# Performance work log

Hardware: AMD Instinct MI355X
Metric: run time of the kernel (lower is better)

Reference implementation:

```python
import jax, jax.numpy as jnp
import numpy as np

# Module hyperparameters (from init_kwargs)
M = 2049          # NpointsMesh (odd)
TAU = 3e-6        # Gaussian spreading width
XLIMS = (0.0, 1.0)
MU0 = 1.0
L = abs(XLIMS[1] - XLIMS[0])
TWO_PI = 2.0 * np.pi
B, N = 16, 512


def _grids():
    kGrid = jnp.asarray(np.linspace(-(M // 2), M // 2, M), jnp.float32)
    xGrid = jnp.asarray(TWO_PI * np.linspace(XLIMS[0], XLIMS[1], M + 1)[:-1] / L, jnp.float32)
    return kGrid, xGrid


def setup_inputs() -> dict:
    key = jax.random.key(0)
    kx, = jax.random.split(key, 1)
    x = jax.random.uniform(kx, (B, N), dtype=jnp.float32)  # points inside xLims
    kGrid, _ = _grids()
    multRe0 = (4.0 * np.pi / (kGrid ** 2 + MU0 ** 2))[None, :].astype(jnp.float32)
    multRe1 = (4.0 * np.pi / (kGrid ** 2 + 1.0))[None, :].astype(jnp.float32)
    zeros = jnp.zeros((1, M), jnp.float32)
    return {"x": x, "multRe0": multRe0, "multIm0": zeros,
            "multRe1": multRe1, "multIm1": zeros}


def reference(x, multRe0, multIm0, multRe1, multIm1):
    kGrid, xGrid = _grids()
    # Gaussian spreading: (B, N, M)
    diff = x[..., None] * (TWO_PI / L) - xGrid
    g = jnp.exp(-(diff * diff) / (4.0 * TAU))
    red = jnp.sum(g, axis=1)  # (B, M)
    # NOTE: tf.signal.fftshift/ifftshift default to ALL axes; jnp matches that default.
    fftG = jnp.fft.fftshift(jnp.fft.fft(jax.lax.complex(red, jnp.zeros_like(red)))) * (L / TWO_PI)
    deconv = jnp.sqrt(np.pi / TAU) * jnp.exp((kGrid ** 2) * TAU)  # (M,) real
    rfft = fftG * deconv
    Re, Im = jnp.real(rfft), jnp.imag(rfft)

    def mix(mRe, mIm):
        # Faithful to source (incl. its naming quirk): real = mRe*Re - mRe*Im,
        # imag = mIm*Re + mIm*Im
        return jax.lax.complex(mRe * Re - mRe * Im, mIm * Re + mIm * Im)

    multFFT = jnp.stack([mix(multRe0, multIm0), mix(multRe1, multIm1)], axis=1)  # (B, 2, M)
    multDeconv = multFFT * deconv  # broadcast over (B, 2, M)
    irfft = jnp.real(jnp.fft.ifft(jnp.fft.ifftshift(multDeconv)))  # (B, 2, M)
    # local = irfft[:,None,:,:] * g[:,:,None,:]; fmm = sum over mesh / M  -> einsum
    fmm = jnp.einsum('bnm,bcm->bnc', g, irfft) / M  # (B, N, 2)
    return fmm
```

## Files before the change

kernel.cpp:

```cpp
#include <hip/hip_runtime.h>
#include <math.h>

#define MM 2049
#define BB 16
#define NN 512
#define JH 1025
#define SPLIT 8
#define CH1 257
#define CH2 129

static constexpr double D_TWO_PI    = 6.283185307179586476925286766559;
static constexpr float  F_TWO_PI    = 6.28318530717958647692f;
static constexpr float  INV_4TAU    = 83333.33333333333f;
static constexpr float  PI_OVER_TAU = 1047197.5511965977f;
static constexpr float  TWO_TAU     = 6.0e-6f;
static constexpr float  INV_2PI     = 0.15915494309189533f;
static constexpr float  INV_M       = 1.0f / 2049.0f;
static constexpr float  WINF        = 8.0f;

#define OFF_CS   0
#define OFF_SN   (OFF_CS + BB * JH)
#define OFF_IRF  (OFF_SN + BB * JH)
#define OFF_RED  (OFF_IRF + BB * 2 * MM)
#define OFF_AB   (OFF_RED + BB * MM)
#define ZERO_FLOATS OFF_RED

__global__ void k_spread(const float* __restrict__ x, float* __restrict__ red) {
    __shared__ float lred[MM];
    __shared__ float lxg[MM];
    const int b = blockIdx.x;
    for (int m = threadIdx.x; m < MM; m += blockDim.x) {
        lred[m] = 0.0f;
        lxg[m]  = (float)(D_TWO_PI * (double)m / (double)MM);
    }
    __syncthreads();
    for (int n = threadIdx.x; n < NN; n += blockDim.x) {
        float xv = x[b * NN + n];
        float xa = xv * F_TWO_PI;
        float p  = xv * (float)MM;
        int m0 = (int)ceilf(p - WINF);  if (m0 < 0) m0 = 0;
        int m1 = (int)floorf(p + WINF); if (m1 > MM - 1) m1 = MM - 1;
        for (int m = m0; m <= m1; ++m) {
            float d = xa - lxg[m];
            float g = expf(-(d * d) * INV_4TAU);
            atomicAdd(&lred[m], g);
        }
    }
    __syncthreads();
    for (int m = threadIdx.x; m < MM; m += blockDim.x)
        red[b * MM + m] = lred[m];
}

__global__ void k_dft1(const float* __restrict__ red,
                       float* __restrict__ CS, float* __restrict__ SN) {
    __shared__ float lred[CH1];
    const int b  = blockIdx.y;
    const int j  = blockIdx.x * blockDim.x + threadIdx.x;
    const int s0 = blockIdx.z * CH1;
    const int s1 = min(s0 + CH1, MM);
    const int cnt = s1 - s0;
    for (int i = threadIdx.x; i < cnt; i += blockDim.x)
        lred[i] = red[b * MM + s0 + i];
    __syncthreads();
    if (j >= JH) return;
    float ct, st;
    {
        float ang = (float)(D_TWO_PI * (double)j / (double)MM);
        __sincosf(ang, &st, &ct);
    }
    float c, s;
    {
        int r0 = (j * s0) % MM;
        float ph = (float)(D_TWO_PI * (double)r0 / (double)MM);
        __sincosf(ph, &s, &c);
    }
    float accc = 0.0f, accs = 0.0f;
    for (int i = 0; i < cnt; ++i) {
        float rv = lred[i];
        accc = fmaf(rv, c, accc);
        accs = fmaf(rv, s, accs);
        float t1 = s * st, t2 = s * ct;
        float cn = fmaf(c, ct, -t1);
        float sn = fmaf(c, st,  t2);
        c = cn; s = sn;
    }
    atomicAdd(&CS[b * JH + j], accc);
    atomicAdd(&SN[b * JH + j], accs);
}

__global__ void k_mid(const float* __restrict__ CS, const float* __restrict__ SN,
                      const float* __restrict__ mRe0, const float* __restrict__ mIm0,
                      const float* __restrict__ mRe1, const float* __restrict__ mIm1,
                      float* __restrict__ AB) {
    const int idx = blockIdx.x * blockDim.x + threadIdx.x;
    if (idx >= BB * JH) return;
    const int b = idx / JH;
    const int j = idx - b * JH;
    const int msh = j + 1024;
    const float jf = (float)j;
    const float d2 = PI_OVER_TAU * expf(jf * jf * TWO_TAU);
    const float fac = (j == 0) ? 1.0f : 2.0f;
    const float sc = INV_2PI * d2 * fac;
    const float csv = CS[idx], snv = SN[idx];
    float4 v;
    v.x =  sc * mRe1[msh] * csv;
    v.y =  sc * mRe0[msh] * csv;
    v.z = -sc * mIm1[msh] * snv;
    v.w = -sc * mIm0[msh] * snv;
    ((float4*)AB)[idx] = v;
}

__global__ void k_dft2(const float* __restrict__ AB, float* __restrict__ irf) {
    __shared__ float4 lab[CH2];
    const int b  = blockIdx.y;
    const int t  = blockIdx.x * blockDim.x + threadIdx.x;
    const int j0 = blockIdx.z * CH2;
    const int j1 = min(j0 + CH2, JH);
    const int cnt = j1 - j0;
    const float4* abg = ((const float4*)AB) + (size_t)b * JH;
    for (int i = threadIdx.x; i < cnt; i += blockDim.x)
        lab[i] = abg[j0 + i];
    __syncthreads();
    if (t >= MM) return;
    float ct, st;
    {
        float ang = (float)(D_TWO_PI * (double)t / (double)MM);
        __sincosf(ang, &st, &ct);
    }
    float c, s;
    {
        int r0 = (t * j0) % MM;
        float ph = (float)(D_TWO_PI * (double)r0 / (double)MM);
        __sincosf(ph, &s, &c);
    }
    float acc0 = 0.0f, acc1 = 0.0f;
    for (int i = 0; i < cnt; ++i) {
        float4 v = lab[i];
        acc0 = fmaf(v.x,  c, acc0);
        acc0 = fmaf(v.z, -s, acc0);
        acc1 = fmaf(v.y,  c, acc1);
        acc1 = fmaf(v.w, -s, acc1);
        float t1 = s * st, t2 = s * ct;
        float cn = fmaf(c, ct, -t1);
        float sn = fmaf(c, st,  t2);
        c = cn; s = sn;
    }
    atomicAdd(&irf[((size_t)b * 2 + 0) * MM + t], acc0 * INV_M);
    atomicAdd(&irf[((size_t)b * 2 + 1) * MM + t], acc1 * INV_M);
}

__global__ void k_gather(const float* __restrict__ x, const float* __restrict__ irf,
                         float* __restrict__ out) {
    const int idx = blockIdx.x * blockDim.x + threadIdx.x;
    if (idx >= BB * NN) return;
    const int b = idx / NN;
    float xv = x[idx];
    float xa = xv * F_TWO_PI;
    float p  = xv * (float)MM;
    int m0 = (int)ceilf(p - WINF);  if (m0 < 0) m0 = 0;
    int m1 = (int)floorf(p + WINF); if (m1 > MM - 1) m1 = MM - 1;
    const float* i0 = irf + ((size_t)b * 2 + 0) * MM;
    const float* i1 = irf + ((size_t)b * 2 + 1) * MM;
    float acc0 = 0.0f, acc1 = 0.0f;
    for (int m = m0; m <= m1; ++m) {
        float xg = (float)(D_TWO_PI * (double)m / (double)MM);
        float d  = xa - xg;
        float g  = expf(-(d * d) * INV_4TAU);
        acc0 = fmaf(g, i0[m], acc0);
        acc1 = fmaf(g, i1[m], acc1);
    }
    out[idx * 2 + 0] = acc0 * INV_M;
    out[idx * 2 + 1] = acc1 * INV_M;
}

extern "C" void kernel_launch(void* const* d_in, const int* in_sizes, int n_in,
                              void* d_out, int out_size, void* d_ws, size_t ws_size,
                              hipStream_t stream) {
    const float* x    = (const float*)d_in[0];
    const float* mRe0 = (const float*)d_in[1];
    const float* mIm0 = (const float*)d_in[2];
    const float* mRe1 = (const float*)d_in[3];
    const float* mIm1 = (const float*)d_in[4];
    float* out = (float*)d_out;

    float* ws  = (float*)d_ws;
    float* CS  = ws + OFF_CS;
    float* SN  = ws + OFF_SN;
    float* irf = ws + OFF_IRF;
    float* red = ws + OFF_RED;
    float* AB  = ws + OFF_AB;

    hipMemsetAsync(ws, 0, (size_t)ZERO_FLOATS * sizeof(float), stream);

    k_spread<<<BB, 256, 0, stream>>>(x, red);
    k_dft1<<<dim3((JH + 255) / 256, BB, SPLIT), 256, 0, stream>>>(red, CS, SN);
    k_mid<<<(BB * JH + 255) / 256, 256, 0, stream>>>(CS, SN, mRe0, mIm0, mRe1, mIm1, AB);
    k_dft2<<<dim3((MM + 255) / 256, BB, SPLIT), 256, 0, stream>>>(AB, irf);
    k_gather<<<(BB * NN + 255) / 256, 256, 0, stream>>>(x, irf, out);
}
```

Measured before the change: 99.58 us.

## Fuse spreading into DFT1 and mid into DFT2, replace atomics with partial buffers

Each k_sdft1 block now spreads the Gaussians only onto its own mesh chunk in shared memory and runs the partial forward DFT directly, writing per-chunk partial sums instead of atomics. k_dft2m sums those partials, applies the deconvolution and multipliers, and runs the inverse DFT, writing per-chunk partial outputs. k_gather then adds those partials up. This removes the memset, two kernel launches and the global atomics, and gives the spread stage more parallelism. In exchange the spread work is repeated for each j-block, and the gather does extra loads.

New measurement: 96.76 us. 1.03x faster.

```diff
diff --git a/kernel.cpp b/kernel.cpp
--- a/kernel.cpp
+++ b/kernel.cpp
@@ -5,11 +5,16 @@
 #define BB 16
 #define NN 512
 #define JH 1025
-#define SPLIT 8
-#define CH1 257
-#define CH2 129
+#define JP 1040
+#define SZ 8
+#define SCH 257
+#define JCH 5
+#define Z2 4
+#define JB 257
+#define TCH 9
 
 static constexpr double D_TWO_PI    = 6.283185307179586476925286766559;
+static constexpr double D_STEP      = D_TWO_PI / 2049.0;
 static constexpr float  F_TWO_PI    = 6.28318530717958647692f;
 static constexpr float  INV_4TAU    = 83333.33333333333f;
 static constexpr float  PI_OVER_TAU = 1047197.5511965977f;
@@ -18,62 +23,36 @@
 static constexpr float  INV_M       = 1.0f / 2049.0f;
 static constexpr float  WINF        = 8.0f;
 
-#define OFF_CS   0
-#define OFF_SN   (OFF_CS + BB * JH)
-#define OFF_IRF  (OFF_SN + BB * JH)
-#define OFF_RED  (OFF_IRF + BB * 2 * MM)
-#define OFF_AB   (OFF_RED + BB * MM)
-#define ZERO_FLOATS OFF_RED
-
-__global__ void k_spread(const float* __restrict__ x, float* __restrict__ red) {
-    __shared__ float lred[MM];
-    __shared__ float lxg[MM];
-    const int b = blockIdx.x;
-    for (int m = threadIdx.x; m < MM; m += blockDim.x) {
-        lred[m] = 0.0f;
-        lxg[m]  = (float)(D_TWO_PI * (double)m / (double)MM);
-    }
+__global__ void k_sdft1(const float* __restrict__ x, float2* __restrict__ PSp) {
+    __shared__ float lred[SCH];
+    __shared__ float lx[NN];
+    const int b  = blockIdx.y;
+    const int z  = blockIdx.z;
+    const int s0 = z * SCH;
+    const int s1 = min(s0 + SCH, MM);
+    const int cnt = s1 - s0;
+    for (int i = threadIdx.x; i < SCH; i += 256) lred[i] = 0.0f;
+    for (int i = threadIdx.x; i < NN;  i += 256) lx[i] = x[b * NN + i];
     __syncthreads();
-    for (int n = threadIdx.x; n < NN; n += blockDim.x) {
-        float xv = x[b * NN + n];
+    for (int n = threadIdx.x; n < NN; n += 256) {
+        float xv = lx[n];
         float xa = xv * F_TWO_PI;
         float p  = xv * (float)MM;
-        int m0 = (int)ceilf(p - WINF);  if (m0 < 0) m0 = 0;
-        int m1 = (int)floorf(p + WINF); if (m1 > MM - 1) m1 = MM - 1;
+        int m0 = (int)ceilf(p - WINF);  if (m0 < s0) m0 = s0;
+        int m1 = (int)floorf(p + WINF); if (m1 > s1 - 1) m1 = s1 - 1;
         for (int m = m0; m <= m1; ++m) {
-            float d = xa - lxg[m];
-            float g = expf(-(d * d) * INV_4TAU);
-            atomicAdd(&lred[m], g);
+            float xg = (float)((double)m * D_STEP);
+            float d  = xa - xg;
+            atomicAdd(&lred[m - s0], expf(-(d * d) * INV_4TAU));
         }
     }
     __syncthreads();
-    for (int m = threadIdx.x; m < MM; m += blockDim.x)
-        red[b * MM + m] = lred[m];
-}
-
-__global__ void k_dft1(const float* __restrict__ red,
-                       float* __restrict__ CS, float* __restrict__ SN) {
-    __shared__ float lred[CH1];
-    const int b  = blockIdx.y;
-    const int j  = blockIdx.x * blockDim.x + threadIdx.x;
-    const int s0 = blockIdx.z * CH1;
-    const int s1 = min(s0 + CH1, MM);
-    const int cnt = s1 - s0;
-    for (int i = threadIdx.x; i < cnt; i += blockDim.x)
-        lred[i] = red[b * MM + s0 + i];
-    __syncthreads();
+    const int j = blockIdx.x * 256 + threadIdx.x;
     if (j >= JH) return;
     float ct, st;
-    {
-        float ang = (float)(D_TWO_PI * (double)j / (double)MM);
-        __sincosf(ang, &st, &ct);
-    }
+    { float ang = (float)((double)j * D_STEP); __sincosf(ang, &st, &ct); }
     float c, s;
-    {
-        int r0 = (j * s0) % MM;
-        float ph = (float)(D_TWO_PI * (double)r0 / (double)MM);
-        __sincosf(ph, &s, &c);
-    }
+    { int r0 = (j * s0) % MM; float ph = (float)((double)r0 * D_STEP); __sincosf(ph, &s, &c); }
     float accc = 0.0f, accs = 0.0f;
     for (int i = 0; i < cnt; ++i) {
         float rv = lred[i];
@@ -84,57 +63,49 @@
         float sn = fmaf(c, st,  t2);
         c = cn; s = sn;
     }
-    atomicAdd(&CS[b * JH + j], accc);
-    atomicAdd(&SN[b * JH + j], accs);
+    PSp[((size_t)b * SZ + z) * JP + j] = make_float2(accc, accs);
 }
 
-__global__ void k_mid(const float* __restrict__ CS, const float* __restrict__ SN,
-                      const float* __restrict__ mRe0, const float* __restrict__ mIm0,
-                      const float* __restrict__ mRe1, const float* __restrict__ mIm1,
-                      float* __restrict__ AB) {
-    const int idx = blockIdx.x * blockDim.x + threadIdx.x;
-    if (idx >= BB * JH) return;
-    const int b = idx / JH;
-    const int j = idx - b * JH;
-    const int msh = j + 1024;
-    const float jf = (float)j;
-    const float d2 = PI_OVER_TAU * expf(jf * jf * TWO_TAU);
-    const float fac = (j == 0) ? 1.0f : 2.0f;
-    const float sc = INV_2PI * d2 * fac;
-    const float csv = CS[idx], snv = SN[idx];
-    float4 v;
-    v.x =  sc * mRe1[msh] * csv;
-    v.y =  sc * mRe0[msh] * csv;
-    v.z = -sc * mIm1[msh] * snv;
-    v.w = -sc * mIm0[msh] * snv;
-    ((float4*)AB)[idx] = v;
-}
-
-__global__ void k_dft2(const float* __restrict__ AB, float* __restrict__ irf) {
-    __shared__ float4 lab[CH2];
-    const int b  = blockIdx.y;
-    const int t  = blockIdx.x * blockDim.x + threadIdx.x;
-    const int j0 = blockIdx.z * CH2;
-    const int j1 = min(j0 + CH2, JH);
-    const int cnt = j1 - j0;
-    const float4* abg = ((const float4*)AB) + (size_t)b * JH;
-    for (int i = threadIdx.x; i < cnt; i += blockDim.x)
-        lab[i] = abg[j0 + i];
+__global__ void k_dft2m(const float2* __restrict__ PSp,
+                        const float* __restrict__ mRe0, const float* __restrict__ mIm0,
+                        const float* __restrict__ mRe1, const float* __restrict__ mIm1,
+                        float* __restrict__ irfp) {
+    __shared__ float4 lab[JB];
+    const int b   = blockIdx.y;
+    const int zj  = blockIdx.z;
+    const int jb0 = zj * JB;
+    const int jb1 = min(jb0 + JB, JH);
+    const int cntj = jb1 - jb0;
+    for (int i = threadIdx.x; i < cntj; i += 256) {
+        const int j = jb0 + i;
+        float cs = 0.0f, sn = 0.0f;
+        const float2* base = PSp + (size_t)b * SZ * JP + j;
+        #pragma unroll
+        for (int z = 0; z < SZ; ++z) {
+            float2 ps = base[(size_t)z * JP];
+            cs += ps.x; sn += ps.y;
+        }
+        const int msh = j + 1024;
+        const float jf = (float)j;
+        const float d2 = PI_OVER_TAU * expf(jf * jf * TWO_TAU);
+        const float fac = (j == 0) ? 1.0f : 2.0f;
+        const float sc = INV_2PI * d2 * fac;
+        float4 v;
+        v.x =  sc * mRe1[msh] * cs;
+        v.y =  sc * mRe0[msh] * cs;
+        v.z = -sc * mIm1[msh] * sn;
+        v.w = -sc * mIm0[msh] * sn;
+        lab[i] = v;
+    }
     __syncthreads();
+    const int t = blockIdx.x * 256 + threadIdx.x;
     if (t >= MM) return;
     float ct, st;
-    {
-        float ang = (float)(D_TWO_PI * (double)t / (double)MM);
-        __sincosf(ang, &st, &ct);
-    }
+    { float ang = (float)((double)t * D_STEP); __sincosf(ang, &st, &ct); }
     float c, s;
-    {
-        int r0 = (t * j0) % MM;
-        float ph = (float)(D_TWO_PI * (double)r0 / (double)MM);
-        __sincosf(ph, &s, &c);
-    }
+    { int r0 = (t * jb0) % MM; float ph = (float)((double)r0 * D_STEP); __sincosf(ph, &s, &c); }
     float acc0 = 0.0f, acc1 = 0.0f;
-    for (int i = 0; i < cnt; ++i) {
+    for (int i = 0; i < cntj; ++i) {
         float4 v = lab[i];
         acc0 = fmaf(v.x,  c, acc0);
         acc0 = fmaf(v.z, -s, acc0);
@@ -142,14 +113,15 @@
         acc1 = fmaf(v.w, -s, acc1);
         float t1 = s * st, t2 = s * ct;
         float cn = fmaf(c, ct, -t1);
-        float sn = fmaf(c, st,  t2);
-        c = cn; s = sn;
+        float sn2 = fmaf(c, st,  t2);
+        c = cn; s = sn2;
     }
-    atomicAdd(&irf[((size_t)b * 2 + 0) * MM + t], acc0 * INV_M);
-    atomicAdd(&irf[((size_t)b * 2 + 1) * MM + t], acc1 * INV_M);
+    float* o = irfp + ((size_t)(zj * BB + b) * 2) * MM + t;
+    o[0]  = acc0 * INV_M;
+    o[MM] = acc1 * INV_M;
 }
 
-__global__ void k_gather(const float* __restrict__ x, const float* __restrict__ irf,
+__global__ void k_gather(const float* __restrict__ x, const float* __restrict__ irfp,
                          float* __restrict__ out) {
     const int idx = blockIdx.x * blockDim.x + threadIdx.x;
     if (idx >= BB * NN) return;
@@ -159,15 +131,20 @@
     float p  = xv * (float)MM;
     int m0 = (int)ceilf(p - WINF);  if (m0 < 0) m0 = 0;
     int m1 = (int)floorf(p + WINF); if (m1 > MM - 1) m1 = MM - 1;
-    const float* i0 = irf + ((size_t)b * 2 + 0) * MM;
-    const float* i1 = irf + ((size_t)b * 2 + 1) * MM;
     float acc0 = 0.0f, acc1 = 0.0f;
     for (int m = m0; m <= m1; ++m) {
-        float xg = (float)(D_TWO_PI * (double)m / (double)MM);
+        float xg = (float)((double)m * D_STEP);
         float d  = xa - xg;
         float g  = expf(-(d * d) * INV_4TAU);
-        acc0 = fmaf(g, i0[m], acc0);
-        acc1 = fmaf(g, i1[m], acc1);
+        float p0 = 0.0f, p1 = 0.0f;
+        #pragma unroll
+        for (int z = 0; z < Z2; ++z) {
+            const float* base = irfp + ((size_t)(z * BB + b) * 2) * MM;
+            p0 += base[m];
+            p1 += base[MM + m];
+        }
+        acc0 = fmaf(g, p0, acc0);
+        acc1 = fmaf(g, p1, acc1);
     }
     out[idx * 2 + 0] = acc0 * INV_M;
     out[idx * 2 + 1] = acc1 * INV_M;
@@ -183,18 +160,10 @@
     const float* mIm1 = (const float*)d_in[4];
     float* out = (float*)d_out;
 
-    float* ws  = (float*)d_ws;
-    float* CS  = ws + OFF_CS;
-    float* SN  = ws + OFF_SN;
-    float* irf = ws + OFF_IRF;
-    float* red = ws + OFF_RED;
-    float* AB  = ws + OFF_AB;
+    float2* PSp = (float2*)d_ws;
+    float*  irfp = (float*)d_ws + (size_t)2 * BB * SZ * JP;
 
-    hipMemsetAsync(ws, 0, (size_t)ZERO_FLOATS * sizeof(float), stream);
-
-    k_spread<<<BB, 256, 0, stream>>>(x, red);
-    k_dft1<<<dim3((JH + 255) / 256, BB, SPLIT), 256, 0, stream>>>(red, CS, SN);
-    k_mid<<<(BB * JH + 255) / 256, 256, 0, stream>>>(CS, SN, mRe0, mIm0, mRe1, mIm1, AB);
-    k_dft2<<<dim3((MM + 255) / 256, BB, SPLIT), 256, 0, stream>>>(AB, irf);
-    k_gather<<<(BB * NN + 255) / 256, 256, 0, stream>>>(x, irf, out);
+    k_sdft1 <<<dim3(JCH, BB, SZ), 256, 0, stream>>>(x, PSp);
+    k_dft2m <<<dim3(TCH, BB, Z2), 256, 0, stream>>>(PSp, mRe0, mIm0, mRe1, mIm1, irfp);
+    k_gather<<<(BB * NN + 255) / 256, 256, 0, stream>>>(x, irfp, out);
 }
```
